# Performance work log

Hardware: AMD Instinct MI355X
Metric: run time of the kernel (lower is better)

## Reference

```python
import jax, jax.numpy as jnp
import numpy as np

ANCHOR_PX = (32, 64, 96, 128)
FIELD = 16.0
POOL, TILES = 2, 3
TAU, NMS_IOU = 0.5, 0.3
MAX_DET = 512
HF, WF, DF = 128, 128, 512
HIDDEN = 1024


def _create_anchors():
    # anchors centered on the field grid, rows ordered (i, j, k): x,y = upper-left, w=h=size
    ii, jj, kk = np.meshgrid(np.arange(HF), np.arange(WF), np.arange(len(ANCHOR_PX)), indexing='ij')
    sz = np.asarray(ANCHOR_PX, np.float32)[kk]
    x = jj * FIELD + FIELD / 2 - sz / 2
    y = ii * FIELD + FIELD / 2 - sz / 2
    return np.stack([x.ravel(), y.ravel(), sz.ravel(), sz.ravel()], axis=1).astype(np.float32)


def setup_inputs() -> dict:
    key = jax.random.key(0)
    ks = jax.random.split(key, 8)
    return {
        'features': jax.random.normal(ks[0], (HF, WF, DF), jnp.float32),
        'rpn_obj': jax.random.normal(ks[1], (HF, WF, 2 * len(ANCHOR_PX)), jnp.float32),
        'rpn_reg': 0.1 * jax.random.normal(ks[2], (HF, WF, 4 * len(ANCHOR_PX)), jnp.float32),
        'anchors': jnp.asarray(_create_anchors()),
        'W1': 0.02 * jax.random.normal(ks[3], (TILES * TILES * DF, HIDDEN), jnp.float32),
        'b1': jnp.zeros((HIDDEN,), jnp.float32),
        'W2': 0.02 * jax.random.normal(ks[4], (HIDDEN, HIDDEN), jnp.float32),
        'b2': jnp.zeros((HIDDEN,), jnp.float32),
        'W3': 0.02 * jax.random.normal(ks[5], (HIDDEN, 4), jnp.float32),
        'b3': jnp.zeros((4,), jnp.float32),
    }


def _map_outputs(output, anchors):
    # faithful port of map_outputs: 3D RPN tensor -> per-anchor rows via gather
    K = len(ANCHOR_PX)
    ap = jnp.asarray(ANCHOR_PX, jnp.float32)
    idx = jnp.argmax(anchors[:, 3:4] == ap[None, :], axis=1).astype(jnp.int32)
    px = ((anchors[:, 0] + anchors[:, 2] / 2) / FIELD).astype(jnp.int32)
    py = ((anchors[:, 1] + anchors[:, 3] / 2) / FIELD).astype(jnp.int32)
    H, W, D = output.shape
    reshaped = output.reshape(H, W, K, D // K)
    return reshaped[py, px, idx]  # (Na, D//K)


def _unparameterize(reg, anchors):
    acx = anchors[:, 0] + anchors[:, 2] / 2
    acy = anchors[:, 1] + anchors[:, 3] / 2
    cx = acx + reg[:, 0] * anchors[:, 2]
    cy = acy + reg[:, 1] * anchors[:, 3]
    w = anchors[:, 2] * jnp.exp(reg[:, 2])
    h = anchors[:, 3] * jnp.exp(reg[:, 3])
    return jnp.stack([cx - w / 2, cy - h / 2, w, h], axis=1)


def _iou_matrix(boxes):
    x1, y1 = boxes[:, 0], boxes[:, 1]
    x2, y2 = x1 + boxes[:, 2], y1 + boxes[:, 3]
    ix = jnp.maximum(0.0, jnp.minimum(x2[:, None], x2[None, :]) - jnp.maximum(x1[:, None], x1[None, :]))
    iy = jnp.maximum(0.0, jnp.minimum(y2[:, None], y2[None, :]) - jnp.maximum(y1[:, None], y1[None, :]))
    inter = ix * iy
    area = boxes[:, 2] * boxes[:, 3]
    return inter / (area[:, None] + area[None, :] - inter + 1e-8)


def _nms_keep(iou, valid, thr):
    # greedy NMS on score-sorted boxes: sequential scan over rows
    n = valid.shape[0]
    rng = jnp.arange(n)
    def step(keep, i):
        suppressed = jnp.any((iou[i] > thr) & keep & (rng < i))
        k = valid[i] & jnp.logical_not(suppressed)
        return keep.at[i].set(k), k
    keep, _ = jax.lax.scan(step, jnp.zeros((n,), bool), rng)
    return keep


def _roialign(features, boxes):
    # pool x pool bilinear samples per tile, tiles x tiles tiles per box, max-pooled per tile
    M = boxes.shape[0]
    T = TILES * POOL
    t = (jnp.arange(T, dtype=jnp.float32) + 0.5) / T
    fx = (boxes[:, 0:1] + t[None, :] * boxes[:, 2:3]) / FIELD - 0.5  # (M, T)
    fy = (boxes[:, 1:2] + t[None, :] * boxes[:, 3:4]) / FIELD - 0.5
    def grid(c, n):
        c = jnp.clip(c, 0.0, n - 1.0)
        c0 = jnp.floor(c).astype(jnp.int32)
        c1 = jnp.minimum(c0 + 1, n - 1)
        return c0, c1, c - c0
    x0, x1, wx = grid(fx, WF)
    y0, y1, wy = grid(fy, HF)
    def g(yi, xi):
        return features[yi[:, :, None], xi[:, None, :]]  # (M, T, T, D)
    wy0, wy1 = (1 - wy)[:, :, None, None], wy[:, :, None, None]
    wx0, wx1 = (1 - wx)[:, None, :, None], wx[:, None, :, None]
    val = g(y0, x0) * wy0 * wx0 + g(y0, x1) * wy0 * wx1 + g(y1, x0) * wy1 * wx0 + g(y1, x1) * wy1 * wx1
    val = val.reshape(M, TILES, POOL, TILES, POOL, DF)
    return jnp.max(val, axis=(2, 4))  # (M, TILES, TILES, D)


def reference(features, rpn_obj, rpn_reg, anchors, W1, b1, W2, b2, W3, b3):
    obj = _map_outputs(rpn_obj, anchors)            # (Na, 2)
    reg = _map_outputs(rpn_reg, anchors)            # (Na, 4)
    scores = jax.nn.softmax(obj, axis=1)[:, 1]      # objectness
    boxes = _unparameterize(reg, anchors)           # proposals (Na, 4)
    # threshold + top-k (fixed-shape surrogate for boolean_mask)
    masked = jnp.where(scores > TAU, scores, -jnp.inf)
    top_scores, top_idx = jax.lax.top_k(masked, MAX_DET)
    valid = jnp.isfinite(top_scores)
    sel = boxes[top_idx]                            # (MAX_DET, 4)
    keep = _nms_keep(_iou_matrix(sel), valid, NMS_IOU)
    # roialign + fast-rcnn refinement head
    pooled = _roialign(features, sel).reshape(MAX_DET, -1)
    h = jax.nn.relu(pooled @ W1 + b1)
    h = jax.nn.relu(h @ W2 + b2)
    deltas = h @ W3 + b3
    refined = _unparameterize(deltas, sel)
    sc = jnp.where(valid, top_scores, 0.0)
    out = jnp.concatenate([refined, sc[:, None]], axis=1)
    return out * keep[:, None].astype(out.dtype)    # (MAX_DET, 5)
```

## Files before the change

### kernel.cpp

```cpp
#include <hip/hip_runtime.h>
#include <math.h>

#define HFD 128
#define WFD 128
#define DFD 512
#define KA  4
#define NA  (HFD*WFD*KA)
#define MAXD 512
#define HID 1024
#define FIN 4608
#define NBUCK 1025
#define BINCAP 64
#define TAUF 0.5f
#define NMS_THR 0.3f
#define SPLITK 4
#define GEMM_BLOCKS (16 * 8 * SPLITK)
#define TBLOCKS ((FIN / 32) * (HID / 32) + (HID / 32) * (HID / 32))

typedef __bf16 bf16x8 __attribute__((ext_vector_type(8)));
typedef float  floatx4 __attribute__((ext_vector_type(4)));

__device__ __forceinline__ unsigned short f2bf(float x) {
    unsigned u = __float_as_uint(x);
    unsigned r = (u + 0x7FFFu + ((u >> 16) & 1u)) >> 16;
    return (unsigned short)r;
}

__device__ __forceinline__ unsigned long long rdlane64(unsigned long long v, int b) {
    unsigned lo = (unsigned)__builtin_amdgcn_readlane((int)(unsigned)v, b);
    unsigned hi = (unsigned)__builtin_amdgcn_readlane((int)(unsigned)(v >> 32), b);
    return ((unsigned long long)hi << 32) | lo;
}

__global__ __launch_bounds__(256)
void front_kernel(const float* __restrict__ rpn_obj,
                  unsigned* __restrict__ hist,
                  unsigned long long* __restrict__ bins) {
    int n = blockIdx.x * 256 + threadIdx.x;
    float2 o = ((const float2*)rpn_obj)[n];
    float m  = fmaxf(o.x, o.y);
    float e0 = expf(o.x - m), e1 = expf(o.y - m);
    float s  = e1 / (e0 + e1);
    if (s > TAUF) {
        unsigned bits = __float_as_uint(s);
        unsigned bk = (bits - 0x3F000000u) >> 13;
        unsigned slot = atomicAdd(&hist[bk], 1u);
        if (slot < BINCAP)
            bins[bk * BINCAP + slot] =
                ((unsigned long long)bits << 32) |
                (unsigned long long)(~(unsigned)n);
    }
}

__global__ __launch_bounds__(1024)
void tgs_kernel(const unsigned* __restrict__ hist,
                const unsigned long long* __restrict__ bins,
                const float* __restrict__ rpn_reg,
                const float* __restrict__ anchors,
                float* __restrict__ sel,
                float* __restrict__ top_score,
                unsigned* __restrict__ valid_g) {
    __shared__ unsigned long long keys[1024];
    __shared__ unsigned Hs[NBUCK];
    __shared__ unsigned wsum[16];
    __shared__ unsigned cntS;
    __shared__ unsigned thrS;

    int tid = threadIdx.x;
    int wave = tid >> 6, lane = tid & 63;

    if (tid == 0) cntS = 0u;
    for (int i = tid; i < NBUCK; i += 1024) Hs[i] = hist[i];
    __syncthreads();
    unsigned sfx = Hs[tid + 1];
#pragma unroll
    for (int d = 1; d < 64; d <<= 1) {
        unsigned v = __shfl_down(sfx, d);
        if (lane + d < 64) sfx += v;
    }
    if (lane == 0) wsum[wave] = sfx;
    __syncthreads();
    if (wave == 0) {
        unsigned orig = (lane < 16) ? wsum[lane] : 0u;
        unsigned s = orig;
#pragma unroll
        for (int d = 1; d < 16; d <<= 1) {
            unsigned v = __shfl_down(s, d);
            if (lane + d < 64) s += v;
        }
        if (lane < 16) wsum[lane] = s - orig;
    }
    __syncthreads();
    unsigned above = wsum[wave];
    unsigned Scur = sfx + above;
    unsigned nx = __shfl_down(Scur, 1);
    unsigned Snxt = (lane == 63) ? above : nx;
    if (tid == 0 && Scur < MAXD) thrS = 0u;
    if (Scur >= MAXD && Snxt < MAXD) thrS = (unsigned)(tid + 1);
    __syncthreads();
    unsigned thr = thrS;

    for (int b = (int)thr + wave; b < NBUCK; b += 16) {
        unsigned c = Hs[b]; if (c > BINCAP) c = BINCAP;
        unsigned base = 0;
        if (lane == 0 && c > 0) base = atomicAdd(&cntS, c);
        base = __shfl(base, 0);
        if (c > 0 && lane < c && base + lane < 1024)
            keys[base + lane] = bins[(long)b * BINCAP + lane];
    }
    __syncthreads();
    unsigned cnt = cntS; if (cnt > 1024) cnt = 1024;
    if (tid >= (int)cnt) keys[tid] = 0ULL;
    __syncthreads();

    unsigned long long k64 = keys[tid];
#pragma unroll
    for (int k = 2; k <= 1024; k <<= 1) {
        for (int j = k >> 1; j >= 64; j >>= 1) {
            keys[tid] = k64;
            __syncthreads();
            unsigned long long v = keys[tid ^ j];
            bool takemax = (((tid & j) == 0) == ((tid & k) == 0));
            k64 = takemax ? (k64 >= v ? k64 : v) : (k64 <= v ? k64 : v);
            __syncthreads();
        }
        int js = ((k >> 1) < 32) ? (k >> 1) : 32;
        for (int j = js; j >= 1; j >>= 1) {
            unsigned lo = __shfl_xor((unsigned)k64, j);
            unsigned hi = __shfl_xor((unsigned)(k64 >> 32), j);
            unsigned long long v = ((unsigned long long)hi << 32) | lo;
            bool takemax = (((tid & j) == 0) == ((tid & k) == 0));
            k64 = takemax ? (k64 >= v ? k64 : v) : (k64 <= v ? k64 : v);
        }
    }

    if (tid < MAXD) {
        unsigned sbits = (unsigned)(k64 >> 32);
        bool v = (sbits != 0u);
        unsigned idx = v ? (unsigned)(~(unsigned)k64) : 0u;
        int cell = idx >> 2, kk = idx & 3;
        float4 rg = *(const float4*)&rpn_reg[cell * 16 + 4 * kk];
        float4 an = *(const float4*)&anchors[idx * 4];
        float acx = an.x + an.z * 0.5f;
        float acy = an.y + an.w * 0.5f;
        float cx = acx + rg.x * an.z;
        float cy = acy + rg.y * an.w;
        float w  = an.z * expf(rg.z);
        float h  = an.w * expf(rg.w);
        ((float4*)sel)[tid] = make_float4(cx - 0.5f * w, cy - 0.5f * h, w, h);
        top_score[tid] = v ? __uint_as_float(sbits) : 0.0f;
        valid_g[tid]   = v ? 1u : 0u;
    }
}

__global__ __launch_bounds__(256)
void roialign_iou_kernel(const float* __restrict__ feat,
                         const float* __restrict__ sel,
                         unsigned short* __restrict__ pooled,
                         unsigned long long* __restrict__ mask,
                         const float* __restrict__ W1,
                         unsigned short* __restrict__ W1t,
                         const float* __restrict__ W2,
                         unsigned short* __restrict__ W2t) {
    __shared__ float tile[32][33];
    int blk = blockIdx.x;
    if (blk >= MAXD * 9 + MAXD) {
        int b = blk - (MAXD * 9 + MAXD);
        const float* W; unsigned short* Wt; int K, N;
        if (b < (FIN / 32) * (HID / 32)) { W = W1; Wt = W1t; K = FIN; N = HID; }
        else { b -= (FIN / 32) * (HID / 32); W = W2; Wt = W2t; K = HID; N = HID; }
        int bn = (b & (N / 32 - 1)) * 32;
        int bk = (b / (N / 32)) * 32;
        int tx = threadIdx.x & 31, ty = threadIdx.x >> 5;
#pragma unroll
        for (int r = 0; r < 32; r += 8)
            tile[ty + r][tx] = W[(long)(bk + ty + r) * N + bn + tx];
        __syncthreads();
#pragma unroll
        for (int r = 0; r < 32; r += 8)
            Wt[(long)(bn + ty + r) * K + bk + tx] = f2bf(tile[tx][ty + r]);
        return;
    }
    if (blk >= MAXD * 9) {
        int i = blk - MAXD * 9;
        int t = threadIdx.x, wv = t >> 6, lane = t & 63;
        float4 bi = ((const float4*)sel)[i];
        float x2i = bi.x + bi.z, y2i = bi.y + bi.w;
        float ai = bi.z * bi.w;
#pragma unroll
        for (int h = 0; h < 2; ++h) {
            int j = h * 256 + wv * 64 + lane;
            float4 bj = ((const float4*)sel)[j];
            float x2j = bj.x + bj.z, y2j = bj.y + bj.w;
            float aj = bj.z * bj.w;
            float ix = fmaxf(0.0f, fminf(x2i, x2j) - fmaxf(bi.x, bj.x));
            float iy = fmaxf(0.0f, fminf(y2i, y2j) - fmaxf(bi.y, bj.y));
            float inter = ix * iy;
            float iou = inter / (ai + aj - inter + 1e-8f);
            unsigned long long bal = __ballot(iou > NMS_THR);
            if (lane == 0) mask[i * 8 + h * 4 + wv] = bal;
        }
        return;
    }
    int mrow = blk / 9;
    int tl = blk - mrow * 9;
    int tp = tl / 3, tq = tl - tp * 3;
    int c = threadIdx.x;
    float4 b = ((const float4*)sel)[mrow];
    float vmax0 = -INFINITY, vmax1 = -INFINITY;
#pragma unroll
    for (int dp = 0; dp < 2; ++dp) {
        int p = tp * 2 + dp;
        float fy = (b.y + ((float)p + 0.5f) / 6.0f * b.w) / 16.0f - 0.5f;
        fy = fminf(fmaxf(fy, 0.0f), 127.0f);
        int y0 = (int)floorf(fy);
        int y1 = min(y0 + 1, 127);
        float wy = fy - (float)y0;
#pragma unroll
        for (int dq = 0; dq < 2; ++dq) {
            int q = tq * 2 + dq;
            float fx = (b.x + ((float)q + 0.5f) / 6.0f * b.z) / 16.0f - 0.5f;
            fx = fminf(fmaxf(fx, 0.0f), 127.0f);
            int x0 = (int)floorf(fx);
            int x1 = min(x0 + 1, 127);
            float wx = fx - (float)x0;
            const float* f00 = feat + (y0 * WFD + x0) * DFD;
            const float* f01 = feat + (y0 * WFD + x1) * DFD;
            const float* f10 = feat + (y1 * WFD + x0) * DFD;
            const float* f11 = feat + (y1 * WFD + x1) * DFD;
            float w00 = (1.0f - wy) * (1.0f - wx);
            float w01 = (1.0f - wy) * wx;
            float w10 = wy * (1.0f - wx);
            float w11 = wy * wx;
            float v0 = f00[c] * w00 + f01[c] * w01 + f10[c] * w10 + f11[c] * w11;
            float v1 = f00[c + 256] * w00 + f01[c + 256] * w01 +
                       f10[c + 256] * w10 + f11[c + 256] * w11;
            vmax0 = fmaxf(vmax0, v0);
            vmax1 = fmaxf(vmax1, v1);
        }
    }
    pooled[mrow * FIN + tl * DFD + c] = f2bf(vmax0);
    pooled[mrow * FIN + tl * DFD + c + 256] = f2bf(vmax1);
}

#define LDK 64
__device__ __forceinline__ int swz(int row, int cs) {
    return row * LDK + (cs ^ ((row & 7) << 3));
}
__global__ __launch_bounds__(256)
void mfma_gemm_kernel(const unsigned short* __restrict__ A,
                      const unsigned short* __restrict__ Bt,
                      float* __restrict__ Cpart,
                      int K,
                      const unsigned long long* __restrict__ mask,
                      const unsigned* __restrict__ valid,
                      unsigned* __restrict__ keep) {
    int blk = blockIdx.x;
    if (blk >= GEMM_BLOCKS) {
        int lane = threadIdx.x;
        if (lane >= 64) return;
        unsigned long long vb[8];
#pragma unroll
        for (int g = 0; g < 8; ++g)
            vb[g] = __ballot(valid[g * 64 + lane] != 0u);
        unsigned long long cw[8], cwn[8];
#pragma unroll
        for (int g = 0; g < 8; ++g)
            cw[g] = mask[(g * 64 + lane) * 8 + 0];
        unsigned supp8 = 0u;
#pragma unroll
        for (int G = 0; G < 8; ++G) {
            if (G < 7) {
#pragma unroll
                for (int g = 0; g < 8; ++g)
                    cwn[g] = mask[(g * 64 + lane) * 8 + (G + 1)];
            }
            unsigned long long alive =
                vb[G] & ~__ballot((supp8 >> G) & 1u);
            unsigned long long Kw = 0ULL;
            while (alive) {
                int b = __builtin_ctzll(alive);
                Kw |= 1ULL << b;
                unsigned long long row = rdlane64(cw[G], b);
                alive &= ~row;
                alive &= ~(1ULL << b);
            }
            keep[G * 64 + lane] = (unsigned)((Kw >> lane) & 1ULL);
#pragma unroll
            for (int g = 0; g < 8; ++g) {
                supp8 |= ((cw[g] & Kw) != 0ULL ? 1u : 0u) << g;
                cw[g] = cwn[g];
            }
        }
        return;
    }

    __shared__ unsigned short As[64 * LDK];
    __shared__ unsigned short Bs[64 * LDK];
    int tid = threadIdx.x;
    int wave = tid >> 6, lane = tid & 63;
    int bz = blk >> 7;
    int rem = blk & 127;
    int bm = (rem >> 4) * 64, bn = (rem & 15) * 64;
    int KC = K / SPLITK;
    int ks = bz * KC;

    floatx4 acc[4] = {};
    int lr = tid >> 2;
    int lk = (tid & 3) << 4;
    int frow = lane & 15, quad = lane >> 4;

    const unsigned short* Ap = A + (long)(bm + lr) * K + lk;
    const unsigned short* Bp = Bt + (long)(bn + lr) * K + lk;
    int ra = wave * 16 + frow;

    for (int k0 = ks; k0 < ks + KC; k0 += 64) {
        uint4 a0 = *(const uint4*)(Ap + k0);
        uint4 a1 = *(const uint4*)(Ap + k0 + 8);
        uint4 b0 = *(const uint4*)(Bp + k0);
        uint4 b1 = *(const uint4*)(Bp + k0 + 8);
        *(uint4*)&As[swz(lr, lk)] = a0;
        *(uint4*)&As[swz(lr, lk + 8)] = a1;
        *(uint4*)&Bs[swz(lr, lk)] = b0;
        *(uint4*)&Bs[swz(lr, lk + 8)] = b1;
        __syncthreads();
        bf16x8 af0 = *(const bf16x8*)&As[swz(ra, quad * 8)];
        bf16x8 af1 = *(const bf16x8*)&As[swz(ra, 32 + quad * 8)];
#pragma unroll
        for (int t = 0; t < 4; ++t) {
            int rb = t * 16 + frow;
            bf16x8 b0v = *(const bf16x8*)&Bs[swz(rb, quad * 8)];
            bf16x8 b1v = *(const bf16x8*)&Bs[swz(rb, 32 + quad * 8)];
            acc[t] = __builtin_amdgcn_mfma_f32_16x16x32_bf16(af0, b0v, acc[t], 0, 0, 0);
            acc[t] = __builtin_amdgcn_mfma_f32_16x16x32_bf16(af1, b1v, acc[t], 0, 0, 0);
        }
        __syncthreads();
    }

    float* Cp = Cpart + (long)bz * MAXD * HID;
#pragma unroll
    for (int t = 0; t < 4; ++t) {
#pragma unroll
        for (int r = 0; r < 4; ++r) {
            int m = bm + wave * 16 + quad * 4 + r;
            int n = bn + t * 16 + frow;
            Cp[(long)m * HID + n] = acc[t][r];
        }
    }
}

__global__ __launch_bounds__(256)
void reduce_bias_relu_kernel(const float* __restrict__ Cpart,
                             const float* __restrict__ bias,
                             unsigned short* __restrict__ out_bf,
                             int MN, int N) {
    int i4 = (blockIdx.x * blockDim.x + threadIdx.x) * 4;
    if (i4 >= MN) return;
    float4 s = *(const float4*)&Cpart[i4];
#pragma unroll
    for (int z = 1; z < SPLITK; ++z) {
        float4 p = *(const float4*)&Cpart[(long)z * MN + i4];
        s.x += p.x; s.y += p.y; s.z += p.z; s.w += p.w;
    }
    int n = i4 & (N - 1);
    float4 bi = *(const float4*)&bias[n];
    s.x = fmaxf(s.x + bi.x, 0.0f);
    s.y = fmaxf(s.y + bi.y, 0.0f);
    s.z = fmaxf(s.z + bi.z, 0.0f);
    s.w = fmaxf(s.w + bi.w, 0.0f);
    uint2 o;
    o.x = (unsigned)f2bf(s.x) | ((unsigned)f2bf(s.y) << 16);
    o.y = (unsigned)f2bf(s.z) | ((unsigned)f2bf(s.w) << 16);
    *(uint2*)&out_bf[i4] = o;
}

__global__ __launch_bounds__(256)
void rowhead_kernel(const float* __restrict__ Cpart,
                    const float* __restrict__ b2,
                    const float* __restrict__ W3,
                    const float* __restrict__ b3,
                    const float* __restrict__ sel,
                    const float* __restrict__ top_score,
                    const unsigned* __restrict__ valid,
                    const unsigned* __restrict__ keep,
                    float* __restrict__ out) {
    __shared__ float red[4][4];
    int r = blockIdx.x, t = threadIdx.x;
    int wave = t >> 6, lane = t & 63;
    int c = t * 4;
    const int MN = MAXD * HID;
    float4 s = *(const float4*)&Cpart[(long)r * HID + c];
#pragma unroll
    for (int z = 1; z < SPLITK; ++z) {
        float4 p = *(const float4*)&Cpart[(long)z * MN + (long)r * HID + c];
        s.x += p.x; s.y += p.y; s.z += p.z; s.w += p.w;
    }
    float4 bi = *(const float4*)&b2[c];
    float h[4];
    h[0] = fmaxf(s.x + bi.x, 0.0f);
    h[1] = fmaxf(s.y + bi.y, 0.0f);
    h[2] = fmaxf(s.z + bi.z, 0.0f);
    h[3] = fmaxf(s.w + bi.w, 0.0f);
    float a0 = 0.f, a1 = 0.f, a2 = 0.f, a3 = 0.f;
#pragma unroll
    for (int i = 0; i < 4; ++i) {
        float4 w = *(const float4*)&W3[(c + i) * 4];
        a0 += h[i] * w.x; a1 += h[i] * w.y;
        a2 += h[i] * w.z; a3 += h[i] * w.w;
    }
#pragma unroll
    for (int off = 32; off > 0; off >>= 1) {
        a0 += __shfl_down(a0, off);
        a1 += __shfl_down(a1, off);
        a2 += __shfl_down(a2, off);
        a3 += __shfl_down(a3, off);
    }
    if (lane == 0) {
        red[wave][0] = a0; red[wave][1] = a1;
        red[wave][2] = a2; red[wave][3] = a3;
    }
    __syncthreads();
    if (t == 0) {
        float d0 = red[0][0] + red[1][0] + red[2][0] + red[3][0] + b3[0];
        float d1 = red[0][1] + red[1][1] + red[2][1] + red[3][1] + b3[1];
        float d2 = red[0][2] + red[1][2] + red[2][2] + red[3][2] + b3[2];
        float d3 = red[0][3] + red[1][3] + red[2][3] + red[3][3] + b3[3];
        if (keep[r] != 0u) {
            float4 b = ((const float4*)sel)[r];
            float acx = b.x + 0.5f * b.z;
            float acy = b.y + 0.5f * b.w;
            float cx = acx + d0 * b.z;
            float cy = acy + d1 * b.w;
            float nw = b.z * expf(d2);
            float nh = b.w * expf(d3);
            out[r * 5 + 0] = cx - 0.5f * nw;
            out[r * 5 + 1] = cy - 0.5f * nh;
            out[r * 5 + 2] = nw;
            out[r * 5 + 3] = nh;
            out[r * 5 + 4] = (valid[r] != 0u) ? top_score[r] : 0.0f;
        } else {
            out[r * 5 + 0] = 0.0f;
            out[r * 5 + 1] = 0.0f;
            out[r * 5 + 2] = 0.0f;
            out[r * 5 + 3] = 0.0f;
            out[r * 5 + 4] = 0.0f;
        }
    }
}

extern "C" void kernel_launch(void* const* d_in, const int* in_sizes, int n_in,
                              void* d_out, int out_size, void* d_ws, size_t ws_size,
                              hipStream_t stream) {
    const float* features = (const float*)d_in[0];
    const float* rpn_obj  = (const float*)d_in[1];
    const float* rpn_reg  = (const float*)d_in[2];
    const float* anchors  = (const float*)d_in[3];
    const float* W1 = (const float*)d_in[4];
    const float* b1 = (const float*)d_in[5];
    const float* W2 = (const float*)d_in[6];
    const float* b2 = (const float*)d_in[7];
    const float* W3 = (const float*)d_in[8];
    const float* b3 = (const float*)d_in[9];
    float* out = (float*)d_out;

    char* ws = (char*)d_ws;
    size_t off = 0;
    auto alloc = [&](size_t bytes) {
        char* p = ws + off;
        off += (bytes + 255) & ~(size_t)255;
        return p;
    };
    unsigned* hist      = (unsigned*)alloc(NBUCK * sizeof(unsigned));
    unsigned long long* bins =
        (unsigned long long*)alloc((size_t)NBUCK * BINCAP * 8);
    float*    sel       = (float*)alloc(MAXD * 4 * sizeof(float));
    float*    top_score = (float*)alloc(MAXD * sizeof(float));
    unsigned* valid     = (unsigned*)alloc(MAXD * sizeof(unsigned));
    unsigned* keep      = (unsigned*)alloc(MAXD * sizeof(unsigned));
    unsigned long long* mask = (unsigned long long*)alloc(MAXD * 8 * 8);
    unsigned short* pooled = (unsigned short*)alloc((size_t)MAXD * FIN * 2);
    unsigned short* W1t = (unsigned short*)alloc((size_t)FIN * HID * 2);
    unsigned short* W2t = (unsigned short*)alloc((size_t)HID * HID * 2);
    unsigned short* h1  = (unsigned short*)alloc((size_t)MAXD * HID * 2);
    float*    Cpart     = (float*)alloc((size_t)SPLITK * MAXD * HID * sizeof(float));
    (void)ws_size; (void)in_sizes; (void)n_in; (void)out_size;

    hipMemsetAsync(hist, 0, NBUCK * sizeof(unsigned), stream);
    front_kernel<<<256, 256, 0, stream>>>(rpn_obj, hist, bins);
    tgs_kernel<<<1, 1024, 0, stream>>>(hist, bins, rpn_reg, anchors,
                                       sel, top_score, valid);
    roialign_iou_kernel<<<MAXD * 9 + MAXD + TBLOCKS, 256, 0, stream>>>(
        features, sel, pooled, mask, W1, W1t, W2, W2t);
    const int MN = MAXD * HID;
    mfma_gemm_kernel<<<GEMM_BLOCKS + 1, 256, 0, stream>>>(
        pooled, W1t, Cpart, FIN, mask, valid, keep);
    reduce_bias_relu_kernel<<<MN / 4 / 256, 256, 0, stream>>>(
        Cpart, b1, h1, MN, HID);
    mfma_gemm_kernel<<<GEMM_BLOCKS, 256, 0, stream>>>(
        h1, W2t, Cpart, HID, nullptr, nullptr, nullptr);
    rowhead_kernel<<<MAXD, 256, 0, stream>>>(Cpart, b2, W3, b3, sel,
                                             top_score, valid, keep, out);
}
```

Before: 172.2 us.

## Move weight transpose into single-block top-k kernel and vectorize roialign loads

The W1/W2 bf16 transpose blocks move from the roialign kernel into the top-k/select kernel, which previously ran as a single 1024-thread block. The transpose now overlaps with the serial selection work and fills the otherwise idle GPU. Each extra block handles four 32x32 tiles. RoIAlign now loads float2 and stores packed bf16 pairs, giving wider memory accesses. The tgs kernel's shared memory grows by about 17KB, which may reduce co-residency.

```diff
diff --git a/kernel.cpp b/kernel.cpp
--- a/kernel.cpp
+++ b/kernel.cpp
@@ -16,6 +16,7 @@
 #define SPLITK 4
 #define GEMM_BLOCKS (16 * 8 * SPLITK)
 #define TBLOCKS ((FIN / 32) * (HID / 32) + (HID / 32) * (HID / 32))
+#define MNALL (MAXD * HID)
 
 typedef __bf16 bf16x8 __attribute__((ext_vector_type(8)));
 typedef float  floatx4 __attribute__((ext_vector_type(4)));
@@ -59,14 +60,38 @@
                 const float* __restrict__ anchors,
                 float* __restrict__ sel,
                 float* __restrict__ top_score,
-                unsigned* __restrict__ valid_g) {
+                unsigned* __restrict__ valid_g,
+                const float* __restrict__ W1,
+                unsigned short* __restrict__ W1t,
+                const float* __restrict__ W2,
+                unsigned short* __restrict__ W2t) {
     __shared__ unsigned long long keys[1024];
     __shared__ unsigned Hs[NBUCK];
     __shared__ unsigned wsum[16];
     __shared__ unsigned cntS;
     __shared__ unsigned thrS;
+    __shared__ float tileT[4][32][33];
 
     int tid = threadIdx.x;
+    if (blockIdx.x > 0) {
+        int sub = tid >> 8, ts = tid & 255;
+        int b = (blockIdx.x - 1) * 4 + sub;
+        const float* W; unsigned short* Wt; int K, N;
+        if (b < (FIN / 32) * (HID / 32)) { W = W1; Wt = W1t; K = FIN; N = HID; }
+        else { b -= (FIN / 32) * (HID / 32); W = W2; Wt = W2t; K = HID; N = HID; }
+        int bn = (b & (N / 32 - 1)) * 32;
+        int bk = (b / (N / 32)) * 32;
+        int tx = ts & 31, ty = ts >> 5;
+#pragma unroll
+        for (int r = 0; r < 32; r += 8)
+            tileT[sub][ty + r][tx] = W[(long)(bk + ty + r) * N + bn + tx];
+        __syncthreads();
+#pragma unroll
+        for (int r = 0; r < 32; r += 8)
+            Wt[(long)(bn + ty + r) * K + bk + tx] = f2bf(tileT[sub][tx][ty + r]);
+        return;
+    }
+
     int wave = tid >> 6, lane = tid & 63;
 
     if (tid == 0) cntS = 0u;
@@ -157,30 +182,8 @@
 void roialign_iou_kernel(const float* __restrict__ feat,
                          const float* __restrict__ sel,
                          unsigned short* __restrict__ pooled,
-                         unsigned long long* __restrict__ mask,
-                         const float* __restrict__ W1,
-                         unsigned short* __restrict__ W1t,
-                         const float* __restrict__ W2,
-                         unsigned short* __restrict__ W2t) {
-    __shared__ float tile[32][33];
+                         unsigned long long* __restrict__ mask) {
     int blk = blockIdx.x;
-    if (blk >= MAXD * 9 + MAXD) {
-        int b = blk - (MAXD * 9 + MAXD);
-        const float* W; unsigned short* Wt; int K, N;
-        if (b < (FIN / 32) * (HID / 32)) { W = W1; Wt = W1t; K = FIN; N = HID; }
-        else { b -= (FIN / 32) * (HID / 32); W = W2; Wt = W2t; K = HID; N = HID; }
-        int bn = (b & (N / 32 - 1)) * 32;
-        int bk = (b / (N / 32)) * 32;
-        int tx = threadIdx.x & 31, ty = threadIdx.x >> 5;
-#pragma unroll
-        for (int r = 0; r < 32; r += 8)
-            tile[ty + r][tx] = W[(long)(bk + ty + r) * N + bn + tx];
-        __syncthreads();
-#pragma unroll
-        for (int r = 0; r < 32; r += 8)
-            Wt[(long)(bn + ty + r) * K + bk + tx] = f2bf(tile[tx][ty + r]);
-        return;
-    }
     if (blk >= MAXD * 9) {
         int i = blk - MAXD * 9;
         int t = threadIdx.x, wv = t >> 6, lane = t & 63;
@@ -205,9 +208,9 @@
     int mrow = blk / 9;
     int tl = blk - mrow * 9;
     int tp = tl / 3, tq = tl - tp * 3;
-    int c = threadIdx.x;
+    int t = threadIdx.x;
     float4 b = ((const float4*)sel)[mrow];
-    float vmax0 = -INFINITY, vmax1 = -INFINITY;
+    float vx = -INFINITY, vy = -INFINITY;
 #pragma unroll
     for (int dp = 0; dp < 2; ++dp) {
         int p = tp * 2 + dp;
@@ -224,23 +227,23 @@
             int x0 = (int)floorf(fx);
             int x1 = min(x0 + 1, 127);
             float wx = fx - (float)x0;
-            const float* f00 = feat + (y0 * WFD + x0) * DFD;
-            const float* f01 = feat + (y0 * WFD + x1) * DFD;
-            const float* f10 = feat + (y1 * WFD + x0) * DFD;
-            const float* f11 = feat + (y1 * WFD + x1) * DFD;
+            const float2* f00 = (const float2*)(feat + (y0 * WFD + x0) * DFD);
+            const float2* f01 = (const float2*)(feat + (y0 * WFD + x1) * DFD);
+            const float2* f10 = (const float2*)(feat + (y1 * WFD + x0) * DFD);
+            const float2* f11 = (const float2*)(feat + (y1 * WFD + x1) * DFD);
+            float2 v00 = f00[t], v01 = f01[t], v10 = f10[t], v11 = f11[t];
             float w00 = (1.0f - wy) * (1.0f - wx);
             float w01 = (1.0f - wy) * wx;
             float w10 = wy * (1.0f - wx);
             float w11 = wy * wx;
-            float v0 = f00[c] * w00 + f01[c] * w01 + f10[c] * w10 + f11[c] * w11;
-            float v1 = f00[c + 256] * w00 + f01[c + 256] * w01 +
-                       f10[c + 256] * w10 + f11[c + 256] * w11;
-            vmax0 = fmaxf(vmax0, v0);
-            vmax1 = fmaxf(vmax1, v1);
-        }
-    }
-    pooled[mrow * FIN + tl * DFD + c] = f2bf(vmax0);
-    pooled[mrow * FIN + tl * DFD + c + 256] = f2bf(vmax1);
+            float rx = v00.x * w00 + v01.x * w01 + v10.x * w10 + v11.x * w11;
+            float ry = v00.y * w00 + v01.y * w01 + v10.y * w10 + v11.y * w11;
+            vx = fmaxf(vx, rx);
+            vy = fmaxf(vy, ry);
+        }
+    }
+    unsigned o = (unsigned)f2bf(vx) | ((unsigned)f2bf(vy) << 16);
+    *(unsigned*)&pooled[mrow * FIN + tl * DFD + t * 2] = o;
 }
 
 #define LDK 64
@@ -337,7 +340,7 @@
         __syncthreads();
     }
 
-    float* Cp = Cpart + (long)bz * MAXD * HID;
+    float* Cp = Cpart + (long)bz * MNALL;
 #pragma unroll
     for (int t = 0; t < 4; ++t) {
 #pragma unroll
@@ -388,11 +391,10 @@
     int r = blockIdx.x, t = threadIdx.x;
     int wave = t >> 6, lane = t & 63;
     int c = t * 4;
-    const int MN = MAXD * HID;
     float4 s = *(const float4*)&Cpart[(long)r * HID + c];
 #pragma unroll
     for (int z = 1; z < SPLITK; ++z) {
-        float4 p = *(const float4*)&Cpart[(long)z * MN + (long)r * HID + c];
+        float4 p = *(const float4*)&Cpart[(long)z * MNALL + (long)r * HID + c];
         s.x += p.x; s.y += p.y; s.z += p.z; s.w += p.w;
     }
     float4 bi = *(const float4*)&b2[c];
@@ -487,10 +489,11 @@
 
     hipMemsetAsync(hist, 0, NBUCK * sizeof(unsigned), stream);
     front_kernel<<<256, 256, 0, stream>>>(rpn_obj, hist, bins);
-    tgs_kernel<<<1, 1024, 0, stream>>>(hist, bins, rpn_reg, anchors,
-                                       sel, top_score, valid);
-    roialign_iou_kernel<<<MAXD * 9 + MAXD + TBLOCKS, 256, 0, stream>>>(
-        features, sel, pooled, mask, W1, W1t, W2, W2t);
+    tgs_kernel<<<1 + TBLOCKS / 4, 1024, 0, stream>>>(
+        hist, bins, rpn_reg, anchors, sel, top_score, valid,
+        W1, W1t, W2, W2t);
+    roialign_iou_kernel<<<MAXD * 9 + MAXD, 256, 0, stream>>>(
+        features, sel, pooled, mask);
     const int MN = MAXD * HID;
     mfma_gemm_kernel<<<GEMM_BLOCKS + 1, 256, 0, stream>>>(
         pooled, W1t, Cpart, FIN, mask, valid, keep);
```

New measurement: 173.5 us. About the same (+0.7%).
